# Performance work log

Measured on AMD Instinct MI355X. Metric: run time of the kernel, lower is better.

## Reference

```python
import jax, jax.numpy as jnp
import numpy as np

BETA = 0.5
PS = 4  # threshold rank per row, and pooling ratio N//PS


def _getM(att, ps):
    # att: [B, N]. Per-row descending sort; threshold = (ps+1)-th largest value.
    vals = -jnp.sort(-att, axis=1)            # descending sort, [B, N]
    thr = vals[:, ps, None]                   # [B, 1]
    mask = att >= thr                         # [B, N] bool
    return jnp.sum(mask.astype(att.dtype), axis=0)  # [N] counts


def setup_inputs() -> dict:
    key = jax.random.key(0)
    k1, k2, k3, k4 = jax.random.split(key, 4)
    B, N, D = 64, 2048, 512
    return {
        "x": jax.random.normal(k1, (B, N, D), dtype=jnp.float32),
        "y": jax.random.normal(k2, (B, N, N), dtype=jnp.float32),
        "attention": jax.random.normal(k3, (B, N), dtype=jnp.float32),
        "att_off": jax.random.normal(k4, (B, N), dtype=jnp.float32),
    }


def reference(x, y, attention, att_off):
    # attention is already [B, N]; flatten(start_dim=1) is a no-op here.
    M = BETA * _getM(attention, PS) + (1.0 - BETA) * _getM(att_off, PS)  # [N]
    # torch.sort(descending=True) on M; take top N//ps indices.
    top_m = jnp.argsort(-M)[: M.shape[0] // PS]  # [K], K = N//PS
    x_sel = x[:, top_m]                          # [B, K, D]
    y_sel = y[:, top_m][:, :, top_m]             # [B, K, K] (two-stage gather)
    return (x_sel, y_sel, top_m)
```

## Files before the change

### kernel.cpp

```cpp
#include <hip/hip_runtime.h>
#include <math.h>

#define NN 2048
#define BB 64
#define DD 512
#define NSEL 512

__device__ __forceinline__ void insert5(float v, float t[5]) {
  if (v > t[4]) {
    if (v > t[0])      { t[4]=t[3]; t[3]=t[2]; t[2]=t[1]; t[1]=t[0]; t[0]=v; }
    else if (v > t[1]) { t[4]=t[3]; t[3]=t[2]; t[2]=t[1]; t[1]=v; }
    else if (v > t[2]) { t[4]=t[3]; t[3]=t[2]; t[2]=v; }
    else if (v > t[3]) { t[4]=t[3]; t[3]=v; }
    else               { t[4]=v; }
  }
}

__global__ void thr_kernel(const float* __restrict__ att,
                           const float* __restrict__ aoff,
                           float* __restrict__ thr) {
  int blk  = blockIdx.x;
  const float* src = (blk < BB) ? att : aoff;
  int row  = (blk < BB) ? blk : blk - BB;
  int lane = threadIdx.x;

  float t[5] = {-INFINITY, -INFINITY, -INFINITY, -INFINITY, -INFINITY};
  const float* rp = src + (size_t)row * NN;
  #pragma unroll
  for (int k = 0; k < NN / 64; ++k) insert5(rp[lane + 64 * k], t);

  for (int off = 1; off < 64; off <<= 1) {
    float b[5];
    #pragma unroll
    for (int k = 0; k < 5; ++k) b[k] = __shfl_xor(t[k], off, 64);
    float m[5];
    int ia = 0, ib = 0;
    #pragma unroll
    for (int k = 0; k < 5; ++k) {
      float av = t[ia], bv = b[ib];
      bool ta = (av >= bv);
      m[k] = ta ? av : bv;
      ia += ta ? 1 : 0;
      ib += ta ? 0 : 1;
    }
    #pragma unroll
    for (int k = 0; k < 5; ++k) t[k] = m[k];
  }
  if (lane == 0) thr[blk] = t[4];
}

__global__ void mkey_kernel(const float* __restrict__ att,
                            const float* __restrict__ aoff,
                            const float* __restrict__ thr,
                            int* __restrict__ key) {
  int n = blockIdx.x * blockDim.x + threadIdx.x;
  if (n >= NN) return;
  int c = 0;
  #pragma unroll 16
  for (int b = 0; b < BB; ++b) c += (att[(size_t)b * NN + n] >= thr[b]) ? 1 : 0;
  #pragma unroll 16
  for (int b = 0; b < BB; ++b) c += (aoff[(size_t)b * NN + n] >= thr[BB + b]) ? 1 : 0;
  key[n] = c;
}

__global__ void __launch_bounds__(1024)
topm_kernel(const int* __restrict__ key,
            int* __restrict__ top_m,
            float* __restrict__ out_tail) {
  __shared__ int kl[NN];
  __shared__ int chist[32][132];
  __shared__ int htot[132];
  __shared__ int gbase[132];
  int t = threadIdx.x;

  for (int i = t; i < 32 * 132; i += 1024) (&chist[0][0])[i] = 0;
  __syncthreads();

  int k0 = key[t];
  int k1 = key[t + 1024];
  kl[t] = k0;
  kl[t + 1024] = k1;
  int c0 = t >> 6;
  int c1 = 16 + (t >> 6);
  atomicAdd(&chist[c0][k0], 1);
  atomicAdd(&chist[c1][k1], 1);
  __syncthreads();

  if (t < 129) {
    int run = 0;
    #pragma unroll 4
    for (int c = 0; c < 32; ++c) { int v = chist[c][t]; chist[c][t] = run; run += v; }
    htot[t] = run;
  }
  __syncthreads();
  if (t == 0) {
    int acc = 0;
    for (int k = 128; k >= 0; --k) { gbase[k] = acc; acc += htot[k]; }
  }
  __syncthreads();

  int n0 = t, n1 = t + 1024;
  int pre0 = 0;
  for (int j = c0 * 64; j < n0; ++j) pre0 += (kl[j] == k0) ? 1 : 0;
  int pre1 = 0;
  for (int j = c1 * 64; j < n1; ++j) pre1 += (kl[j] == k1) ? 1 : 0;

  int r0 = gbase[k0] + chist[c0][k0] + pre0;
  int r1 = gbase[k1] + chist[c1][k1] + pre1;
  if (r0 < NSEL) { top_m[r0] = n0; out_tail[r0] = (float)n0; }
  if (r1 < NSEL) { top_m[r1] = n1; out_tail[r1] = (float)n1; }
}

__global__ void gather_kernel(const float* __restrict__ x,
                              const float* __restrict__ y,
                              const int* __restrict__ top_m,
                              float* __restrict__ xs,
                              float* __restrict__ ys) {
  __shared__ float row[NN];
  __shared__ int cols[NSEL];
  int blk = blockIdx.x;
  int b = blk >> 9;
  int i = blk & (NSEL - 1);
  int t = threadIdx.x;

  int r = top_m[i];

  const float4* src = (const float4*)(y + (size_t)b * NN * NN + (size_t)r * NN);
  float4* row4 = (float4*)row;
  row4[t]       = src[t];
  row4[t + 256] = src[t + 256];

  for (int j = t; j < NSEL; j += 256) cols[j] = top_m[j];

  if (t < 128) {
    const float4* xsrc = (const float4*)(x + ((size_t)b * NN + r) * DD);
    float4*       xdst = (float4*)(xs + ((size_t)b * NSEL + i) * DD);
    xdst[t] = xsrc[t];
  }
  __syncthreads();

  float* dst = ys + ((size_t)b * NSEL + i) * DD;
  dst[t]       = row[cols[t]];
  dst[t + 256] = row[cols[t + 256]];
}

extern "C" void kernel_launch(void* const* d_in, const int* in_sizes, int n_in,
                              void* d_out, int out_size, void* d_ws, size_t ws_size,
                              hipStream_t stream) {
  const float* x    = (const float*)d_in[0];
  const float* y    = (const float*)d_in[1];
  const float* att  = (const float*)d_in[2];
  const float* aoff = (const float*)d_in[3];

  float* out = (float*)d_out;
  float* xs   = out;
  float* ysel = out + (size_t)BB * NSEL * DD;
  float* tail = ysel + (size_t)BB * NSEL * NSEL;

  float* thr   = (float*)d_ws;
  int*   key   = (int*)d_ws + 128;
  int*   top_m = (int*)d_ws + 128 + NN;

  hipLaunchKernelGGL(thr_kernel, dim3(2 * BB), dim3(64), 0, stream, att, aoff, thr);
  hipLaunchKernelGGL(mkey_kernel, dim3(NN / 256), dim3(256), 0, stream, att, aoff, thr, key);
  hipLaunchKernelGGL(topm_kernel, dim3(1), dim3(1024), 0, stream, key, top_m, tail);
  hipLaunchKernelGGL(gather_kernel, dim3(BB * NSEL), dim3(256), 0, stream, x, y, top_m, xs, ysel);
}
```

Baseline: 130.1 us.

## Process multiple rows per block with double-buffered y row prefetch in gather

The gather kernel now handles 8 selected rows per block instead of one. It keeps two shared-memory row buffers so the next y row is loaded into registers while the current row's columns are gathered. It also writes the output as float2 and loads the column index table once per block rather than once per row. The aim is to overlap global loads with the gather and spread the per-block setup cost over more rows. The trade-off is 8x fewer blocks (4096), which lowers the parallelism available to hide memory latency, and larger shared-memory use per block.

```diff
diff --git a/kernel.cpp b/kernel.cpp
--- a/kernel.cpp
+++ b/kernel.cpp
@@ -5,6 +5,7 @@
 #define BB 64
 #define DD 512
 #define NSEL 512
+#define IPB 8
 
 __device__ __forceinline__ void insert5(float v, float t[5]) {
   if (v > t[4]) {
@@ -111,37 +112,67 @@
   if (r1 < NSEL) { top_m[r1] = n1; out_tail[r1] = (float)n1; }
 }
 
-__global__ void gather_kernel(const float* __restrict__ x,
-                              const float* __restrict__ y,
-                              const int* __restrict__ top_m,
-                              float* __restrict__ xs,
-                              float* __restrict__ ys) {
-  __shared__ float row[NN];
+__global__ void __launch_bounds__(256)
+gather_kernel(const float* __restrict__ x,
+              const float* __restrict__ y,
+              const int* __restrict__ top_m,
+              float* __restrict__ xs,
+              float* __restrict__ ys) {
+  __shared__ float row[2][NN];
   __shared__ int cols[NSEL];
   int blk = blockIdx.x;
-  int b = blk >> 9;
-  int i = blk & (NSEL - 1);
-  int t = threadIdx.x;
-
-  int r = top_m[i];
-
-  const float4* src = (const float4*)(y + (size_t)b * NN * NN + (size_t)r * NN);
-  float4* row4 = (float4*)row;
-  row4[t]       = src[t];
-  row4[t + 256] = src[t + 256];
+  int b  = blk >> 6;
+  int i0 = (blk & 63) * IPB;
+  int t  = threadIdx.x;
 
   for (int j = t; j < NSEL; j += 256) cols[j] = top_m[j];
 
-  if (t < 128) {
-    const float4* xsrc = (const float4*)(x + ((size_t)b * NN + r) * DD);
-    float4*       xdst = (float4*)(xs + ((size_t)b * NSEL + i) * DD);
-    xdst[t] = xsrc[t];
-  }
-  __syncthreads();
-
-  float* dst = ys + ((size_t)b * NSEL + i) * DD;
-  dst[t]       = row[cols[t]];
-  dst[t + 256] = row[cols[t + 256]];
+  const float* ybase = y + (size_t)b * NN * NN;
+
+  float4 pre0, pre1;
+  {
+    int r = top_m[i0];
+    const float4* src = (const float4*)(ybase + (size_t)r * NN);
+    pre0 = src[t];
+    pre1 = src[t + 256];
+  }
+  {
+    float4* b0 = (float4*)row[0];
+    b0[t]       = pre0;
+    b0[t + 256] = pre1;
+  }
+  __syncthreads();
+
+  #pragma unroll
+  for (int k = 0; k < IPB; ++k) {
+    int cur = k & 1;
+    if (k + 1 < IPB) {
+      int rn = top_m[i0 + k + 1];
+      const float4* src = (const float4*)(ybase + (size_t)rn * NN);
+      pre0 = src[t];
+      pre1 = src[t + 256];
+    }
+    int rk = top_m[i0 + k];
+    if (t < 128) {
+      const float4* xsrc = (const float4*)(x + ((size_t)b * NN + rk) * DD);
+      float4*       xdst = (float4*)(xs + ((size_t)b * NSEL + (i0 + k)) * DD);
+      xdst[t] = xsrc[t];
+    }
+    {
+      const float* rw = row[cur];
+      float2 o;
+      o.x = rw[cols[2 * t]];
+      o.y = rw[cols[2 * t + 1]];
+      float2* dst = (float2*)(ys + ((size_t)b * NSEL + (i0 + k)) * DD);
+      dst[t] = o;
+    }
+    if (k + 1 < IPB) {
+      float4* bn = (float4*)row[cur ^ 1];
+      bn[t]       = pre0;
+      bn[t + 256] = pre1;
+    }
+    __syncthreads();
+  }
 }
 
 extern "C" void kernel_launch(void* const* d_in, const int* in_sizes, int n_in,
@@ -164,5 +195,6 @@
   hipLaunchKernelGGL(thr_kernel, dim3(2 * BB), dim3(64), 0, stream, att, aoff, thr);
   hipLaunchKernelGGL(mkey_kernel, dim3(NN / 256), dim3(256), 0, stream, att, aoff, thr, key);
   hipLaunchKernelGGL(topm_kernel, dim3(1), dim3(1024), 0, stream, key, top_m, tail);
-  hipLaunchKernelGGL(gather_kernel, dim3(BB * NSEL), dim3(256), 0, stream, x, y, top_m, xs, ysel);
-}
+  hipLaunchKernelGGL(gather_kernel, dim3(BB * (NSEL / IPB)), dim3(256), 0, stream,
+                     x, y, top_m, xs, ysel);
+}
```

After: 136.4 us. +4.8%, slower.

## Restructure gather into per-wave multi-row kernel with register prefetch and nontemporal IO

Applied to the files above, without the earlier changes.

Reworks the gather kernel so each wave handles 8 selected rows, keeping its own LDS row buffer and prefetching the next y row into registers while the current one is gathered. It uses nontemporal loads and stores and writes gathered columns as float4 instead of scalars, and loads the column index table once per block instead of once per row. The grid drops from 32768 to 1024 blocks, which cuts per-block overhead but lowers parallelism and adds register and LDS pressure. mkey_kernel is relaunched with 64-thread blocks to spread it over more blocks.

```diff
diff --git a/kernel.cpp b/kernel.cpp
--- a/kernel.cpp
+++ b/kernel.cpp
@@ -5,6 +5,8 @@
 #define BB 64
 #define DD 512
 #define NSEL 512
+
+typedef float fx4 __attribute__((ext_vector_type(4)));
 
 __device__ __forceinline__ void insert5(float v, float t[5]) {
   if (v > t[4]) {
@@ -53,7 +55,7 @@
                             const float* __restrict__ aoff,
                             const float* __restrict__ thr,
                             int* __restrict__ key) {
-  int n = blockIdx.x * blockDim.x + threadIdx.x;
+  int n = blockIdx.x * 64 + threadIdx.x;
   if (n >= NN) return;
   int c = 0;
   #pragma unroll 16
@@ -111,37 +113,73 @@
   if (r1 < NSEL) { top_m[r1] = n1; out_tail[r1] = (float)n1; }
 }
 
-__global__ void gather_kernel(const float* __restrict__ x,
-                              const float* __restrict__ y,
-                              const int* __restrict__ top_m,
-                              float* __restrict__ xs,
-                              float* __restrict__ ys) {
-  __shared__ float row[NN];
+__global__ void __launch_bounds__(256)
+gather_kernel(const float* __restrict__ x,
+              const float* __restrict__ y,
+              const int* __restrict__ top_m,
+              float* __restrict__ xs,
+              float* __restrict__ ys) {
+  __shared__ float rowbuf[4][NN];
   __shared__ int cols[NSEL];
+  int t = threadIdx.x;
+  int w = t >> 6, lane = t & 63;
   int blk = blockIdx.x;
-  int b = blk >> 9;
-  int i = blk & (NSEL - 1);
-  int t = threadIdx.x;
-
-  int r = top_m[i];
-
-  const float4* src = (const float4*)(y + (size_t)b * NN * NN + (size_t)r * NN);
-  float4* row4 = (float4*)row;
-  row4[t]       = src[t];
-  row4[t + 256] = src[t + 256];
-
-  for (int j = t; j < NSEL; j += 256) cols[j] = top_m[j];
-
-  if (t < 128) {
-    const float4* xsrc = (const float4*)(x + ((size_t)b * NN + r) * DD);
-    float4*       xdst = (float4*)(xs + ((size_t)b * NSEL + i) * DD);
-    xdst[t] = xsrc[t];
-  }
-  __syncthreads();
-
-  float* dst = ys + ((size_t)b * NSEL + i) * DD;
-  dst[t]       = row[cols[t]];
-  dst[t + 256] = row[cols[t + 256]];
+  int b = blk >> 4;
+  int iblk = blk & 15;
+
+  cols[t]       = top_m[t];
+  cols[t + 256] = top_m[t + 256];
+  __syncthreads();
+
+  float* myrow = rowbuf[w];
+  int i0 = iblk * 32 + w * 8;
+  const float* ybase = y + (size_t)b * NN * NN;
+
+  fx4 pr[8];
+  {
+    int r = cols[i0];
+    const fx4* src = (const fx4*)(ybase + (size_t)r * NN);
+    #pragma unroll
+    for (int j = 0; j < 8; ++j)
+      pr[j] = __builtin_nontemporal_load(&src[lane + 64 * j]);
+  }
+
+  #pragma unroll
+  for (int k = 0; k < 8; ++k) {
+    int i = i0 + k;
+    {
+      fx4* mb = (fx4*)myrow;
+      #pragma unroll
+      for (int j = 0; j < 8; ++j) mb[lane + 64 * j] = pr[j];
+    }
+    if (k < 7) {
+      int rn = cols[i + 1];
+      const fx4* src = (const fx4*)(ybase + (size_t)rn * NN);
+      #pragma unroll
+      for (int j = 0; j < 8; ++j)
+        pr[j] = __builtin_nontemporal_load(&src[lane + 64 * j]);
+    }
+    {
+      int r = cols[i];
+      const fx4* xsrc = (const fx4*)(x + ((size_t)b * NN + r) * DD);
+      fx4*       xdst = (fx4*)(xs + ((size_t)b * NSEL + i) * DD);
+      #pragma unroll
+      for (int j = 0; j < 2; ++j) {
+        fx4 v = __builtin_nontemporal_load(&xsrc[lane + 64 * j]);
+        __builtin_nontemporal_store(v, &xdst[lane + 64 * j]);
+      }
+    }
+    {
+      float o[8];
+      #pragma unroll
+      for (int j = 0; j < 8; ++j) o[j] = myrow[cols[8 * lane + j]];
+      fx4* dst = (fx4*)(ys + ((size_t)b * NSEL + i) * DD);
+      fx4 o0 = {o[0], o[1], o[2], o[3]};
+      fx4 o1 = {o[4], o[5], o[6], o[7]};
+      __builtin_nontemporal_store(o0, &dst[2 * lane]);
+      __builtin_nontemporal_store(o1, &dst[2 * lane + 1]);
+    }
+  }
 }
 
 extern "C" void kernel_launch(void* const* d_in, const int* in_sizes, int n_in,
@@ -162,7 +200,8 @@
   int*   top_m = (int*)d_ws + 128 + NN;
 
   hipLaunchKernelGGL(thr_kernel, dim3(2 * BB), dim3(64), 0, stream, att, aoff, thr);
-  hipLaunchKernelGGL(mkey_kernel, dim3(NN / 256), dim3(256), 0, stream, att, aoff, thr, key);
+  hipLaunchKernelGGL(mkey_kernel, dim3(32), dim3(64), 0, stream, att, aoff, thr, key);
   hipLaunchKernelGGL(topm_kernel, dim3(1), dim3(1024), 0, stream, key, top_m, tail);
-  hipLaunchKernelGGL(gather_kernel, dim3(BB * NSEL), dim3(256), 0, stream, x, y, top_m, xs, ysel);
-}
+  hipLaunchKernelGGL(gather_kernel, dim3(BB * 16), dim3(256), 0, stream,
+                     x, y, top_m, xs, ysel);
+}
```

Measured after the change: 129.8 us. No clear change (-0.2%).
